# Performance work log

Hardware: AMD Instinct MI355X
Metric: run time of the kernel (lower is better)

## Reference

```python
import jax, jax.numpy as jnp
import numpy as np
from jax import lax

EPS = 1e-31
V, L, B, T = 30000, 400, 16, 145
E, EH, DH, ENC, COMB = 100, 150, 200, 300, 500
SOS = 1


def setup_inputs() -> dict:
    key = jax.random.key(0)
    ks = jax.random.split(key, 32)
    def p(i, shape):
        return jax.random.normal(ks[i], shape, dtype=jnp.float32) * 0.05
    return {
        "input_tensor": jax.random.randint(ks[0], (L, B), 0, V),
        "embedding": p(1, (V, E)),
        "enc_Wih_f": p(2, (3 * EH, E)), "enc_Whh_f": p(3, (3 * EH, EH)),
        "enc_bih_f": p(4, (3 * EH,)), "enc_bhh_f": p(5, (3 * EH,)),
        "enc_Wih_b": p(6, (3 * EH, E)), "enc_Whh_b": p(7, (3 * EH, EH)),
        "enc_bih_b": p(8, (3 * EH,)), "enc_bhh_b": p(9, (3 * EH,)),
        "adapter_W": p(10, (DH, ENC)), "adapter_b": p(11, (DH,)),
        "dec_Wih": p(12, (3 * DH, E)), "dec_Whh": p(13, (3 * DH, DH)),
        "dec_bih": p(14, (3 * DH,)), "dec_bhh": p(15, (3 * DH,)),
        "bil_W": p(16, (1, DH, ENC)), "bil_b": p(17, (1,)),
        "cover_weight": jax.random.uniform(ks[18], (1,), dtype=jnp.float32),
        "ptr_W": p(19, (1, COMB)), "ptr_b": p(20, (1,)),
        "preout_W": p(21, (E, COMB)), "preout_b": p(22, (E,)),
        "out_b": p(23, (V,)),
    }


def _gru_cell(x, h, Wih, Whh, bih, bhh):
    # torch GRU cell semantics (gates ordered r, z, n)
    gi = x @ Wih.T + bih
    gh = h @ Whh.T + bhh
    ir, iz, i_n = jnp.split(gi, 3, axis=-1)
    hr, hz, hn = jnp.split(gh, 3, axis=-1)
    r = jax.nn.sigmoid(ir + hr)
    z = jax.nn.sigmoid(iz + hz)
    n = jnp.tanh(i_n + r * hn)
    return (1.0 - z) * n + z * h


def _run_gru(emb, Wih, Whh, bih, bhh):
    # emb: [L, B, E] -> outputs [L, B, H], final hidden [B, H]
    h0 = jnp.zeros((emb.shape[1], Whh.shape[1]), emb.dtype)
    def step(h, x):
        h = _gru_cell(x, h, Wih, Whh, bih, bhh)
        return h, h
    hT, ys = lax.scan(step, h0, emb)
    return ys, hT


def reference(input_tensor, embedding,
              enc_Wih_f, enc_Whh_f, enc_bih_f, enc_bhh_f,
              enc_Wih_b, enc_Whh_b, enc_bih_b, enc_bhh_b,
              adapter_W, adapter_b,
              dec_Wih, dec_Whh, dec_bih, dec_bhh,
              bil_W, bil_b, cover_weight,
              ptr_W, ptr_b, preout_W, preout_b, out_b):
    # ----- encoder: bidirectional single-layer GRU -----
    emb = embedding[input_tensor]                       # [L, B, E]
    out_f, h_f = _run_gru(emb, enc_Wih_f, enc_Whh_f, enc_bih_f, enc_bhh_f)
    out_r, h_b = _run_gru(emb[::-1], enc_Wih_b, enc_Whh_b, enc_bih_b, enc_bhh_b)
    enc_out = jnp.concatenate([out_f, out_r[::-1]], axis=-1)   # [L, B, 300]
    enc_hidden = jnp.concatenate([h_f, h_b], axis=-1)          # [B, 300]
    h0 = enc_hidden @ adapter_W.T + adapter_b                  # enc_dec_adapter -> [B, 200]

    enc_word_idx = input_tensor.T                              # [B, L]
    batch_idx = jnp.arange(enc_out.shape[1])[:, None]

    # ----- decoder: greedy loop with enc attention + coverage + pointer-gen -----
    def dec_step(carry, _):
        h, cover, tok = carry
        x = embedding[tok]                                     # [B, E]
        h = _gru_cell(x, h, dec_Wih, dec_Whh, dec_bih, dec_bhh)
        # bilinear energy: h W e + b, plus coverage term
        hW = h @ bil_W[0]                                      # [B, 300]
        energy = jnp.einsum('be,lbe->lb', hW, enc_out) + bil_b[0]
        energy = energy + cover_weight[0] * jnp.log(cover.T + EPS)
        attn = jax.nn.softmax(energy, axis=0)                  # [L, B], softmax over enc steps
        context = jnp.einsum('lbe,lb->be', enc_out, attn)      # [B, 300]
        combined = jnp.concatenate([h, context], axis=-1)      # [B, 500]
        pre = combined @ preout_W.T + preout_b                 # [B, 100]
        logits = pre @ embedding.T + out_b                     # tied output embedding [B, V]
        p_ptr = jax.nn.sigmoid(combined @ ptr_W.T + ptr_b)     # [B, 1]
        gen = jax.nn.softmax(logits, axis=1)
        attn_bl = attn.T                                       # [B, L]
        out = (1.0 - p_ptr) * gen
        out = out.at[batch_idx, enc_word_idx].add(p_ptr * attn_bl)
        new_tok = jnp.argmax(out, axis=1)
        return (h, cover + attn_bl, new_tok), out

    cover0 = jnp.zeros(enc_word_idx.shape, emb.dtype)
    tok0 = jnp.full((enc_out.shape[1],), SOS, dtype=input_tensor.dtype)
    _, outputs = lax.scan(dec_step, (h0, cover0, tok0), None, length=T)
    return outputs  # [T, B, V] pointer-generator mixture probabilities
```

## Files before the change

### kernel.cpp

```cpp
#include <hip/hip_runtime.h>

namespace {

constexpr int Vv=30000, Ll=400, Bb=16, Tt=145;
constexpr int Ee=100, EHh=150, DHh=200, ENc=300;
constexpr int SOS_TOK=1;
constexpr int NB=256, NT=512;

constexpr long SO_EMB = 0;
constexpr long SO_GIF = SO_EMB + 6400L*100;
constexpr long SO_GIB = SO_GIF + 6400L*450;
constexpr long SO_ENC = SO_GIB + 6400L*450;
constexpr long SO_WCAT= SO_GIF;

constexpr long OFF_M    = 0;
constexpr long OFF_N    = OFF_M + 6400L*200;
constexpr long OFF_Q    = OFF_N + 6400L*100;
constexpr long OFF_HENC = OFF_Q + 6400;
constexpr long OFF_HDEC = OFF_HENC + 2L*16*150;
constexpr long OFF_COVER= OFF_HDEC + 2L*16*200;
constexpr long OFF_EXPE = OFF_COVER + 6400;
constexpr long OFF_CTXP = OFF_EXPE + 2L*6400;
constexpr long OFF_PRE  = OFF_CTXP + 2L*16*8*104;
constexpr long OFF_PPTR = OFF_PRE + 2L*16*100;
constexpr long OFF_ZATT = OFF_PPTR + 32;
constexpr long OFF_PSUM = OFF_ZATT + 32;
constexpr long OFF_CAND = OFF_PSUM + 2L*4096;
constexpr long WS_F32_END = OFF_CAND + 2L*16*400*2;
constexpr long PMAX_BYTE = ((WS_F32_END*4 + 255)/256)*256;
constexpr long IWS_BYTE  = PMAX_BYTE + 2L*4096*8;
constexpr int ISVL=0, IGV=6400, IGLS=12800, ICG0=19216, INGR=23328;
constexpr long BAR_BYTE  = ((IWS_BYTE + 23344L*4 + 255)/256)*256;
constexpr int HB_CNT=0, HB_GEN=32, EP_H=64, EP_CTX=96, EP_PRE=128, EP_S4=160, ABRT=192;

struct Args {
  const int* itok;
  const float* emb;
  const float* Wfih; const float* Wfhh; const float* bfih; const float* bfhh;
  const float* Wbih; const float* Wbhh; const float* bbih; const float* bbhh;
  const float* adW; const float* adb;
  const float* dWih; const float* dWhh; const float* dbih; const float* dbhh;
  const float* bilW; const float* bilb; const float* cw;
  const float* ptrW; const float* ptrb;
  const float* preW; const float* preb; const float* outb;
  float* out; float* ws; unsigned long long* pmax; int* iws; int* bar;
};

__device__ __forceinline__ int chunkStart(int c){ return c*117 + (c<48? c:48); }
__device__ __forceinline__ int chunkSize(int c){ return 117 + (c<48?1:0); }
__device__ __forceinline__ float sigm(float x){ return 1.f/(1.f+expf(-x)); }
__device__ __forceinline__ unsigned long long packvi(float val, int v){
  return ((unsigned long long)__float_as_uint(val)<<32) | (unsigned)(~(unsigned)v);
}
__device__ __forceinline__ float ald(const float* p){
  return __hip_atomic_load(p, __ATOMIC_RELAXED, __HIP_MEMORY_SCOPE_AGENT); }
__device__ __forceinline__ void ast(float* p, float v){
  __hip_atomic_store(p, v, __ATOMIC_RELAXED, __HIP_MEMORY_SCOPE_AGENT); }
__device__ __forceinline__ unsigned long long aldu(const unsigned long long* p){
  return __hip_atomic_load(p, __ATOMIC_RELAXED, __HIP_MEMORY_SCOPE_AGENT); }
__device__ __forceinline__ void astu(unsigned long long* p, unsigned long long v){
  __hip_atomic_store(p, v, __ATOMIC_RELAXED, __HIP_MEMORY_SCOPE_AGENT); }
__device__ __forceinline__ int aldi(const int* p){
  return __hip_atomic_load(p, __ATOMIC_RELAXED, __HIP_MEMORY_SCOPE_AGENT); }

#define CTXP_PTR(par,b,g2,k) (a.ws + OFF_CTXP + (((long)(par)*16+(b))*8+(g2))*104 + (k))

__device__ __forceinline__ void hbar(int* bar){
  __syncthreads();
  if (threadIdx.x==0){
    int* cnt=bar+HB_CNT; int* gen=bar+HB_GEN; int* abrt=bar+ABRT;
    if (aldi(abrt)==0){
      __builtin_amdgcn_fence(__ATOMIC_RELEASE, "agent");
      int g = aldi(gen);
      int arr = __hip_atomic_fetch_add(cnt, 1, __ATOMIC_RELAXED, __HIP_MEMORY_SCOPE_AGENT);
      if (arr == NB-1){
        __hip_atomic_store(cnt, 0, __ATOMIC_RELAXED, __HIP_MEMORY_SCOPE_AGENT);
        __hip_atomic_fetch_add(gen, 1, __ATOMIC_RELEASE, __HIP_MEMORY_SCOPE_AGENT);
      } else {
        long it=0;
        while (aldi(gen) == g){
          __builtin_amdgcn_s_sleep(2);
          if (++it > 3000000L){ __hip_atomic_store(abrt,1,__ATOMIC_RELAXED,__HIP_MEMORY_SCOPE_AGENT); break; }
          if ((it&1023)==0 && aldi(abrt)!=0) break;
        }
      }
      __builtin_amdgcn_fence(__ATOMIC_ACQUIRE, "agent");
    }
  }
  __syncthreads();
}

__device__ __forceinline__ void waitEp(int* ep, int target, int* abrt){
  if (threadIdx.x==0){
    if (aldi(abrt)==0){
      long it=0;
      while (aldi(ep) < target){
        __builtin_amdgcn_s_sleep(1);
        if (++it > 3000000L){ __hip_atomic_store(abrt,1,__ATOMIC_RELAXED,__HIP_MEMORY_SCOPE_AGENT); break; }
        if ((it&2047)==0 && aldi(abrt)!=0) break;
      }
    }
  }
  __syncthreads();
}
__device__ __forceinline__ void bumpEp(int* ep){
  __syncthreads();
  if (threadIdx.x==0){
    asm volatile("s_waitcnt vmcnt(0) lgkmcnt(0)" ::: "memory");
    __hip_atomic_fetch_add(ep, 1, __ATOMIC_RELAXED, __HIP_MEMORY_SCOPE_AGENT);
  }
}

__device__ void sortB(const Args& a, int b, char* smem){
  int tid=threadIdx.x;
  int* key=(int*)smem;
  key[tid] = (tid<Ll)? (a.itok[tid*16+b]*Ll + tid) : 0x7FFFFFFF;
  __syncthreads();
  for (int k=2;k<=512;k<<=1){
    for (int j=k>>1;j>0;j>>=1){
      int ixj = tid^j;
      if (ixj>tid){
        int x=key[tid], y=key[ixj];
        bool up = ((tid&k)==0);
        if ((x>y)==up){ key[tid]=y; key[ixj]=x; }
      }
      __syncthreads();
    }
  }
  int* ngS=(int*)(smem+2048);
  if (tid==0){
    int* svl=a.iws+ISVL+b*400; int* gvv=a.iws+IGV+b*400;
    int* gls=a.iws+IGLS+b*401;
    int ng=0, prev=-1;
    for (int i=0;i<400;i++){
      int kk=key[i]; int tok=kk/400, l=kk-tok*400;
      svl[i]=l;
      if (tok!=prev){ gvv[ng]=tok; gls[ng]=i; ng++; prev=tok; }
    }
    gls[ng]=400;
    a.iws[INGR+b]=ng;
    ngS[0]=ng;
  }
  __syncthreads();
  int ng=ngS[0];
  const int* gvv=a.iws+IGV+b*400;
  for (int c=tid;c<=256;c+=NT){
    int target=(c<256)? chunkStart(c) : 0x7FFFFFFF;
    int lo=0,hi=ng;
    while(lo<hi){ int mid=(lo+hi)>>1; if (gvv[mid]<target) lo=mid+1; else hi=mid; }
    a.iws[ICG0+b*257+c]=lo;
  }
}

template<int MODE>
__device__ void tileGemm(const Args& a, char* smem){
  float* Xl=(float*)smem;
  float* Wl=(float*)(smem+25600);
  const int K   = MODE? 300 : 100;
  const int NC  = MODE? 301 : 900;
  const int nCT = MODE? 5 : 15;
  const int nTiles = 100*nCT;
  const float* X = a.out + (MODE? SO_ENC : SO_EMB);
  int ty=threadIdx.x>>4, tx=threadIdx.x&15;
  for (int tile=blockIdx.x; tile<nTiles; tile+=NB){
    int rt=tile%100, ct=tile/100;
    int r0=rt*64, c0=ct*64;
    float acc[2][4];
    #pragma unroll
    for (int i=0;i<2;i++){
      #pragma unroll
      for (int j=0;j<4;j++) acc[i][j]=0.f;
    }
    for (int k0=0;k0<K;k0+=100){
      for (int i=threadIdx.x;i<1600;i+=NT){
        int rr=i/25, e4=i%25;
        ((float4*)Xl)[rr*25+e4] = *((const float4*)(X + (long)(r0+rr)*K + k0) + e4);
      }
      for (int i=threadIdx.x;i<1600;i+=NT){
        int rr=i/25, e4=i%25; int c=c0+rr;
        float4 w={0.f,0.f,0.f,0.f};
        if (c<NC){
          const float* wr;
          if (MODE==0) wr = (c<450)? (a.Wfih + (long)c*100) : (a.Wbih + (long)(c-450)*100);
          else         wr = a.out + SO_WCAT + (long)c*300 + k0;
          w = *((const float4*)wr + e4);
        }
        ((float4*)Wl)[rr*25+e4]=w;
      }
      __syncthreads();
      for (int k4=0;k4<25;k4++){
        float4 a4[2], b4[4];
        #pragma unroll
        for (int i=0;i<2;i++) a4[i]=((float4*)Xl)[(ty*2+i)*25+k4];
        #pragma unroll
        for (int j=0;j<4;j++) b4[j]=((float4*)Wl)[(tx*4+j)*25+k4];
        #pragma unroll
        for (int i=0;i<2;i++){
          #pragma unroll
          for (int j=0;j<4;j++){
            acc[i][j] += a4[i].x*b4[j].x;
            acc[i][j] += a4[i].y*b4[j].y;
            acc[i][j] += a4[i].z*b4[j].z;
            acc[i][j] += a4[i].w*b4[j].w;
          }
        }
      }
      __syncthreads();
    }
    #pragma unroll
    for (int i=0;i<2;i++){
      #pragma unroll
      for (int j=0;j<4;j++){
        int r=r0+ty*2+i, c=c0+tx*4+j;
        if (c<NC){
          if (MODE==0){
            int dir=c/450, cc=c-dir*450;
            float v=acc[i][j] + (dir? a.bbih : a.bfih)[cc];
            a.out[(dir?SO_GIB:SO_GIF) + (long)r*450 + cc]=v;
          } else {
            if (c<200)      a.ws[OFF_M + (long)r*200 + c]=acc[i][j];
            else if (c<300) a.ws[OFF_N + (long)r*100 + (c-200)]=acc[i][j];
            else            a.ws[OFF_Q + r]=acc[i][j];
          }
        }
      }
    }
  }
}

__device__ void encoderPhase(const Args& a, int bid, char* smem){
  int tid=threadIdx.x;
  int dir=bid>>4, b=bid&15;
  float* hbuf=(float*)smem;
  float* gbuf=(float*)(smem+2048);
  float* pacc=(float*)(smem+8192);
  const float* Whh = dir? a.Wbhh : a.Wfhh;
  const float* bhh = dir? a.bbhh : a.bfhh;
  const float* giBase = a.out + (dir? SO_GIB : SO_GIF);
  int ks=tid/150; int j=tid-ks*150;
  bool act = (ks<3);
  float w[3][50];
  if (act){
    #pragma unroll
    for (int g=0;g<3;g++)
      for (int k=0;k<50;k++)
        w[g][k]=Whh[(long)(g*150+j)*150 + ks*50 + k];
  }
  float b0=0,b1=0,b2=0;
  if (act && ks==0){ b0=bhh[j]; b1=bhh[150+j]; b2=bhh[300+j]; }
  for (int i=tid;i<192;i+=NT) hbuf[i]=0.f;
  {
    int l0 = dir? 399 : 0;
    for (int i=tid;i<450;i+=NT) gbuf[i]=giBase[((long)l0*16+b)*450+i];
  }
  __syncthreads();
  for (int s=0;s<400;s++){
    int p=s&1;
    int l=dir? 399-s : s;
    if (tid>=450 && s+1<400){
      int ln=dir? 399-(s+1) : s+1;
      for (int i=tid-450;i<450;i+=62) gbuf[(p^1)*452+i]=giBase[((long)ln*16+b)*450+i];
    }
    if (act){
      float ar=0.f, az=0.f, an=0.f;
      const float* hr=hbuf + p*192 + ks*64;
      #pragma unroll
      for (int k4=0;k4<12;k4++){
        float4 h4=*(const float4*)(hr + k4*4);
        ar+=h4.x*w[0][k4*4+0]; ar+=h4.y*w[0][k4*4+1]; ar+=h4.z*w[0][k4*4+2]; ar+=h4.w*w[0][k4*4+3];
        az+=h4.x*w[1][k4*4+0]; az+=h4.y*w[1][k4*4+1]; az+=h4.z*w[1][k4*4+2]; az+=h4.w*w[1][k4*4+3];
        an+=h4.x*w[2][k4*4+0]; an+=h4.y*w[2][k4*4+1]; an+=h4.z*w[2][k4*4+2]; an+=h4.w*w[2][k4*4+3];
      }
      {
        float h48=hr[48], h49=hr[49];
        ar+=h48*w[0][48]+h49*w[0][49];
        az+=h48*w[1][48]+h49*w[1][49];
        an+=h48*w[2][48]+h49*w[2][49];
      }
      pacc[(ks*3+0)*152+j]=ar;
      pacc[(ks*3+1)*152+j]=az;
      pacc[(ks*3+2)*152+j]=an;
    }
    __syncthreads();
    if (act && ks==0){
      float ar=pacc[(0*3+0)*152+j]+pacc[(1*3+0)*152+j]+pacc[(2*3+0)*152+j];
      float az=pacc[(0*3+1)*152+j]+pacc[(1*3+1)*152+j]+pacc[(2*3+1)*152+j];
      float an=pacc[(0*3+2)*152+j]+pacc[(1*3+2)*152+j]+pacc[(2*3+2)*152+j];
      const float* gi=gbuf + p*452;
      float r=sigm(gi[j]      + ar + b0);
      float z=sigm(gi[150+j]  + az + b1);
      float n=tanhf(gi[300+j] + r*(an + b2));
      int slot=(j/50)*64 + (j%50);
      float hold=hbuf[p*192+slot];
      float hv=(1.f-z)*n + z*hold;
      hbuf[(p^1)*192+slot]=hv;
      a.out[SO_ENC + ((long)l*16+b)*300 + dir*150 + j]=hv;
      if (s==399) a.ws[OFF_HENC + ((long)dir*16+b)*150 + j]=hv;
    }
    __syncthreads();
  }
}

__device__ void s1Phase(const Args& a, int bid, int t, char* smem){
  int tid=threadIdx.x;
  int q=t&1, p1=q^1;
  float* xw=(float*)smem;
  float* hw=(float*)(smem+6400);
  int* tokL=(int*)(smem+19200);
  if (t==0){
    if (tid<16) tokL[tid]=SOS_TOK;
  } else {
    int b=tid>>5, ln=tid&31;
    float zs=0.f;
    for (int c=ln;c<256;c+=32) zs+=ald(&a.ws[OFF_PSUM + ((long)p1*256+c)*16 + b]);
    #pragma unroll
    for (int off=16;off;off>>=1) zs+=__shfl_xor(zs,off,32);
    float Z=zs;
    unsigned long long best=0;
    for (int c=ln;c<256;c+=32){
      unsigned long long pm=aldu(&a.pmax[((long)p1*256+c)*16+b]);
      float ev=__uint_as_float((unsigned)(pm>>32));
      int v=(int)(~(unsigned)(pm & 0xFFFFFFFFull));
      unsigned long long pk=packvi(ev/Z, v);
      if (pk>best) best=pk;
    }
    int ng=a.iws[INGR+b];
    const float* cd=a.ws+OFF_CAND + ((long)p1*16+b)*800;
    const int* gvv=a.iws+IGV+b*400;
    for (int g=ln;g<ng;g+=32){
      float v1=ald(&cd[g*2]), v2=ald(&cd[g*2+1]);
      unsigned long long pk=packvi(v1/Z + v2, gvv[g]);
      if (pk>best) best=pk;
    }
    #pragma unroll
    for (int off=16;off;off>>=1){
      unsigned long long o=__shfl_xor(best,off,32);
      if (o>best) best=o;
    }
    if (ln==0) tokL[b]=(int)(~(unsigned)(best & 0xFFFFFFFFull));
  }
  __syncthreads();
  for (int i=tid;i<1600;i+=NT){ int b=i/100, e=i-b*100; xw[i]=a.emb[(long)tokL[b]*100+e]; }
  for (int i=tid;i<3200;i+=NT) hw[i]=ald(&a.ws[OFF_HDEC + (long)p1*3200 + i]);
  __syncthreads();
  int pair=tid>>3, lane=tid&7;
  int uj=pair>>4, b=pair&15;
  int j=bid*4+uj;
  float air=0,aiz=0,ain=0,ahr=0,ahz=0,ahn=0;
  const float* x=xw+b*100;
  for (int k=lane;k<100;k+=8){
    float xv=x[k];
    air+=xv*a.dWih[(long)j*100+k];
    aiz+=xv*a.dWih[(long)(200+j)*100+k];
    ain+=xv*a.dWih[(long)(400+j)*100+k];
  }
  const float* h=hw+b*200;
  for (int k=lane;k<200;k+=8){
    float hv=h[k];
    ahr+=hv*a.dWhh[(long)j*200+k];
    ahz+=hv*a.dWhh[(long)(200+j)*200+k];
    ahn+=hv*a.dWhh[(long)(400+j)*200+k];
  }
  #pragma unroll
  for (int off=4;off;off>>=1){
    air+=__shfl_xor(air,off,8); aiz+=__shfl_xor(aiz,off,8); ain+=__shfl_xor(ain,off,8);
    ahr+=__shfl_xor(ahr,off,8); ahz+=__shfl_xor(ahz,off,8); ahn+=__shfl_xor(ahn,off,8);
  }
  if (lane==0){
    float r=sigm(air + a.dbih[j]     + ahr + a.dbhh[j]);
    float z=sigm(aiz + a.dbih[200+j] + ahz + a.dbhh[200+j]);
    float n=tanhf(ain + a.dbih[400+j] + r*(ahn + a.dbhh[400+j]));
    ast(&a.ws[OFF_HDEC + (long)q*3200 + b*200 + j], (1.f-z)*n + z*h[j]);
  }
}

__device__ void s2ePhase(const Args& a, int idx, int t, char* smem){
  int tid=threadIdx.x;
  int q=t&1, p1=q^1;
  int b=idx&15, lg=idx>>4, l0=lg*50;
  float* hb =(float*)smem;
  float* exl=(float*)(smem+1024);
  float* zpS=(float*)(smem+1280);
  for (int i=tid;i<200;i+=NT) hb[i]=ald(&a.ws[OFF_HDEC + (long)q*3200 + b*200 + i]);
  if (tid==0){
    float zp=0.f;
    if (t>0){
      #pragma unroll
      for (int g2=0;g2<8;g2++) zp+=ald(CTXP_PTR(p1,b,g2,101));
    }
    zpS[0]=zp;
  }
  __syncthreads();
  int unit=tid>>3, lane=tid&7;
  if (unit<50){
    int l=l0+unit;
    const float* Mr=a.ws+OFF_M + (long)(l*16+b)*200;
    float acc=0.f;
    for (int k=lane;k<200;k+=8) acc+=hb[k]*Mr[k];
    #pragma unroll
    for (int off=4;off;off>>=1) acc+=__shfl_xor(acc,off,8);
    if (lane==0){
      float* cov=a.ws+OFF_COVER + b*400 + l;
      float cv=*cov;
      if (t>0) cv += ald(&a.ws[OFF_EXPE + (long)p1*6400 + l*16 + b]) / zpS[0];
      *cov=cv;
      float en = acc + a.bilb[0] + a.cw[0]*logf(cv + 1e-31f);
      float ex = expf(en);
      ast(&a.ws[OFF_EXPE + (long)q*6400 + l*16 + b], ex);
      exl[unit]=ex;
    }
  }
  __syncthreads();
  int u2=tid>>2, lane2=tid&3;
  if (u2<102){
    int k=u2; float acc=0.f;
    if (k<100){
      for (int ll=lane2;ll<50;ll+=4) acc+=exl[ll]*a.ws[OFF_N + (long)((l0+ll)*16+b)*100 + k];
    } else if (k==100){
      for (int ll=lane2;ll<50;ll+=4) acc+=exl[ll]*a.ws[OFF_Q + (l0+ll)*16 + b];
    } else {
      for (int ll=lane2;ll<50;ll+=4) acc+=exl[ll];
    }
    #pragma unroll
    for (int off=2;off;off>>=1) acc+=__shfl_xor(acc,off,4);
    if (lane2==0) ast(CTXP_PTR(q,b,lg,k), acc);
  }
}

__device__ void preFinal(const Args& a, int b, int t, char* smem, int* bar){
  int tid=threadIdx.x;
  int q=t&1;
  float* hb   =(float*)smem;
  float* prehL=(float*)(smem+1024);
  float* ctxs =(float*)(smem+1536);
  for (int i=tid;i<200;i+=NT) hb[i]=ald(&a.ws[OFF_HDEC + (long)q*3200 + b*200 + i]);
  __syncthreads();
  int unit=tid>>2, lane=tid&3;
  if (unit<101){
    const float* w=(unit<100)? (a.preW + (long)unit*500) : a.ptrW;
    float acc=0.f;
    for (int k=lane;k<200;k+=4) acc+=hb[k]*w[k];
    #pragma unroll
    for (int off=2;off;off>>=1) acc+=__shfl_xor(acc,off,4);
    if (lane==0) prehL[unit]=acc;
  }
  waitEp(bar+EP_CTX, 128*(t+1), bar+ABRT);
  if (tid<408){
    int k=tid>>2, lane2=tid&3;
    float acc=0.f;
    for (int g2=lane2;g2<8;g2+=4) acc+=ald(CTXP_PTR(q,b,g2,k));
    #pragma unroll
    for (int off=2;off;off>>=1) acc+=__shfl_xor(acc,off,4);
    if (lane2==0) ctxs[k]=acc;
  }
  __syncthreads();
  if (tid<100){
    int k=tid;
    ast(&a.ws[OFF_PRE + ((long)q*16+b)*100 + k], ctxs[k]/ctxs[101] + prehL[k] + a.preb[k]);
  }
  if (tid==511){
    float za=ctxs[101];
    ast(&a.ws[OFF_ZATT + (long)q*16 + b], za);
    ast(&a.ws[OFF_PPTR + (long)q*16 + b], sigm(ctxs[100]/za + prehL[100] + a.ptrb[0]));
  }
}

__device__ void wbPhase(const Args& a, int c, int p1, int tr, float* exPrev, char* smem){
  int tid=threadIdx.x;
  int v0=chunkStart(c), nv=chunkSize(c);
  float* zpart=(float*)(smem+8192);
  float* zl1=(float*)(smem+10240);
  float* pp1=(float*)(smem+10304);
  {
    int b=tid&15, seg=tid>>4;
    float z=0.f;
    for (int cc=seg;cc<256;cc+=32) z+=ald(&a.ws[OFF_PSUM + ((long)p1*256+cc)*16 + b]);
    zpart[seg*16+b]=z;
  }
  __syncthreads();
  if (tid<16){
    float z=0.f;
    for (int s2=0;s2<32;s2++) z+=zpart[s2*16+tid];
    zl1[tid]=z;
    pp1[tid]=ald(&a.ws[OFF_PPTR + (long)p1*16 + tid]);
  }
  __syncthreads();
  if (tid<16){
    int b=tid;
    float sc=(1.f-pp1[b])/zl1[b];
    const int* cg0=a.iws+ICG0+b*257; const int* gvv=a.iws+IGV+b*400;
    const float* cd=a.ws+OFF_CAND + ((long)p1*16+b)*800;
    for (int g=cg0[c];g<cg0[c+1];g++){
      int idx=(gvv[g]-v0)*17+b;
      exPrev[idx] += ald(&cd[g*2+1])*(1.f-pp1[b])/sc;
    }
  }
  __syncthreads();
  {
    int tot=nv*16;
    for (int u=tid;u<tot;u+=NT){
      int b2=u/nv, vl=u-b2*nv;
      float sc=(1.f-pp1[b2])/zl1[b2];
      __builtin_nontemporal_store(exPrev[vl*17+b2]*sc,
                                  &a.out[((long)tr*16+b2)*30000 + v0+vl]);
    }
  }
  __syncthreads();
}

__device__ void s4Main(const Args& a, int c, int q, float* exCur, char* smem){
  int tid=threadIdx.x;
  int v0=chunkStart(c), nv=chunkSize(c);
  float* preL=(float*)smem;
  float* ppqL=(float*)(smem+6400);
  float* zaqL=(float*)(smem+6464);
  for (int u=tid;u<1600;u+=NT){
    int b=u/100, k=u-b*100;
    preL[u]=ald(&a.ws[OFF_PRE + ((long)q*16+b)*100 + k]);
  }
  if (tid<16){
    ppqL[tid]=ald(&a.ws[OFF_PPTR + (long)q*16 + tid]);
    zaqL[tid]=ald(&a.ws[OFF_ZATT + (long)q*16 + tid]);
  }
  __syncthreads();
  int bloc=tid&15;
  float4 preg[25];
  {
    const float4* p4=(const float4*)(preL + bloc*100);
    #pragma unroll
    for (int e4=0;e4<25;e4++) preg[e4]=p4[e4];
  }
  int nu=nv*16;
  const float4* emb4=(const float4*)a.emb;
  for (int u=tid;u<nu;u+=NT){
    int vl=u>>4; int v=v0+vl;
    float acc=a.outb[v];
    const float4* er=emb4 + (long)v*25;
    #pragma unroll
    for (int e4=0;e4<25;e4++){
      float4 A=er[e4], Bv=preg[e4];
      acc += A.x*Bv.x + A.y*Bv.y + A.z*Bv.z + A.w*Bv.w;
    }
    exCur[vl*17+bloc]=expf(acc);
  }
  __syncthreads();
  {
    int b=tid>>5, sg=tid&31;
    float s=0.f; unsigned long long m=0;
    for (int vl=sg;vl<nv;vl+=32){
      float ex=exCur[vl*17+b];
      s+=ex;
      unsigned long long pk=packvi(ex, v0+vl);
      if (pk>m) m=pk;
    }
    #pragma unroll
    for (int off=16;off;off>>=1){
      s+=__shfl_xor(s,off,32);
      unsigned long long om=__shfl_xor(m,off,32);
      if (om>m) m=om;
    }
    if (sg==0){
      ast(&a.ws[OFF_PSUM + ((long)q*256+c)*16 + b], s);
      astu(&a.pmax[((long)q*256+c)*16 + b], m);
    }
  }
  if (tid<16){
    int b=tid;
    const int* cg0=a.iws+ICG0+b*257; const int* gvv=a.iws+IGV+b*400;
    const int* gls=a.iws+IGLS+b*401; const int* svl=a.iws+ISVL+b*400;
    float* cd=a.ws+OFF_CAND + ((long)q*16+b)*800;
    float pfac=ppqL[b]/(1.f-ppqL[b]);
    for (int g=cg0[c];g<cg0[c+1];g++){
      int v=gvv[g];
      float gs=0.f;
      for (int i2=gls[g];i2<gls[g+1];i2++) gs+=ald(&a.ws[OFF_EXPE + (long)q*6400 + svl[i2]*16 + b]);
      ast(&cd[g*2],   exCur[(v-v0)*17+b]);
      ast(&cd[g*2+1], pfac*gs/zaqL[b]);
    }
  }
}

__global__ void kInitBar(int* bar){
  int t=threadIdx.x;
  if (t<256) bar[t]=0;
}

__global__ __launch_bounds__(NT,1) void mega(Args a){
  __shared__ __align__(16) char smem[53248];
  int bid=blockIdx.x, tid=threadIdx.x;
  int* bar=a.bar;
  int* abrt=bar+ABRT;
  float* exBuf0=(float*)(smem+36864);
  float* exBuf1=(float*)(smem+44928);

  if (bid<16){
    sortB(a,bid,smem);
  } else {
    for (long i=(long)(bid-16)*NT+tid; i<640000; i+=240L*NT){
      long pair=i/100; int e=(int)(i-pair*100);
      a.out[SO_EMB+i]=a.emb[(long)a.itok[pair]*100+e];
    }
    for (int i=(bid-16)*NT+tid; i<6400; i+=240*NT) a.ws[OFF_COVER+i]=0.f;
  }
  hbar(bar);

  tileGemm<0>(a,smem);
  hbar(bar);

  if (bid<32) encoderPhase(a,bid,smem);
  hbar(bar);

  for (long i=(long)bid*NT+tid; i<90300; i+=(long)NB*NT){
    int rr=(int)(i/300), k=(int)(i-(long)rr*300);
    float v;
    if (rr<200)      v=a.bilW[(long)rr*300+k];
    else if (rr<300) v=a.preW[(long)(rr-200)*500+200+k];
    else             v=a.ptrW[200+k];
    a.out[SO_WCAT+i]=v;
  }
  if (bid>=32 && bid<48){
    int b=bid-32;
    int unit=tid>>1, lane=tid&1;
    if (unit<200){
      int j=unit;
      const float* w=a.adW+(long)j*300 + lane*150;
      const float* hh=a.ws+OFF_HENC + ((long)lane*16+b)*150;
      float acc=0.f;
      for (int e=0;e<150;e++) acc+=hh[e]*w[e];
      acc+=__shfl_xor(acc,1,2);
      if (lane==0) a.ws[OFF_HDEC + 1L*3200 + b*200 + j]=acc + a.adb[j];
    }
  }
  hbar(bar);

  tileGemm<1>(a,smem);
  hbar(bar);

  for (int t=0;t<Tt;t++){
    int q=t&1, p1=q^1;
    float* exPrev = p1? exBuf1 : exBuf0;
    float* exCur  = q?  exBuf1 : exBuf0;
    if (bid<50){
      waitEp(bar+EP_S4, 256*t, abrt);
      s1Phase(a,bid,t,smem);
      bumpEp(bar+EP_H);
    }
    if (t>0) wbPhase(a,bid,p1,t-1,exPrev,smem);
    if (bid>=64 && bid<192){
      waitEp(bar+EP_H, 50*(t+1), abrt);
      s2ePhase(a,bid-64,t,smem);
      bumpEp(bar+EP_CTX);
    }
    if (bid>=240){
      waitEp(bar+EP_H, 50*(t+1), abrt);
      preFinal(a,bid-240,t,smem,bar);
      bumpEp(bar+EP_PRE);
    }
    waitEp(bar+EP_PRE, 16*(t+1), abrt);
    s4Main(a,bid,q,exCur,smem);
    bumpEp(bar+EP_S4);
  }
  waitEp(bar+EP_S4, 256*Tt, abrt);
  wbPhase(a,bid,(Tt-1)&1,Tt-1,((Tt-1)&1)?exBuf1:exBuf0,smem);
}

}

extern "C" void kernel_launch(void* const* d_in, const int* in_sizes, int n_in,
                              void* d_out, int out_size, void* d_ws, size_t ws_size,
                              hipStream_t stream) {
  Args a;
  a.itok=(const int*)d_in[0];
  a.emb =(const float*)d_in[1];
  a.Wfih=(const float*)d_in[2]; a.Wfhh=(const float*)d_in[3];
  a.bfih=(const float*)d_in[4]; a.bfhh=(const float*)d_in[5];
  a.Wbih=(const float*)d_in[6]; a.Wbhh=(const float*)d_in[7];
  a.bbih=(const float*)d_in[8]; a.bbhh=(const float*)d_in[9];
  a.adW =(const float*)d_in[10]; a.adb=(const float*)d_in[11];
  a.dWih=(const float*)d_in[12]; a.dWhh=(const float*)d_in[13];
  a.dbih=(const float*)d_in[14]; a.dbhh=(const float*)d_in[15];
  a.bilW=(const float*)d_in[16]; a.bilb=(const float*)d_in[17];
  a.cw  =(const float*)d_in[18];
  a.ptrW=(const float*)d_in[19]; a.ptrb=(const float*)d_in[20];
  a.preW=(const float*)d_in[21]; a.preb=(const float*)d_in[22];
  a.outb=(const float*)d_in[23];
  a.out =(float*)d_out;
  a.ws  =(float*)d_ws;
  a.pmax=(unsigned long long*)((char*)d_ws + PMAX_BYTE);
  a.iws =(int*)((char*)d_ws + IWS_BYTE);
  a.bar =(int*)((char*)d_ws + BAR_BYTE);

  kInitBar<<<dim3(1),dim3(256),0,stream>>>(a.bar);
  void* kargs[] = { (void*)&a };
  hipLaunchCooperativeKernel(reinterpret_cast<const void*>(mega),
                             dim3(NB), dim3(NT), kargs, 0, stream);
}
```

Baseline: 11.36 ms.

## Replace double-buffered decoder scratch with per-step ring slots and drop preFinal stage

Per-step intermediates (hidden state, exp energies, context partials, psum/pmax, candidates) now go into a ring of per-timestep slots. Most slots live in not-yet-written regions of the output buffer, so they are never overwritten across steps and plain loads can replace relaxed atomic loads. The separate preFinal block group is removed. The pre/ptr projection of h moves into s1, and the context reduction is folded into s4 and wb, which removes one epoch-wait stage from the critical path. It also adds exponential backoff in the spin-wait and relies on reusing output memory as scratch before it is finally written.

Measured after the change: 12.38 ms. 1.09x slower.

```diff
diff --git a/kernel.cpp b/kernel.cpp
--- a/kernel.cpp
+++ b/kernel.cpp
@@ -13,25 +13,28 @@
 constexpr long SO_ENC = SO_GIB + 6400L*450;
 constexpr long SO_WCAT= SO_GIF;
 
+constexpr int RH    = 0;
+constexpr int REXP  = 3200;
+constexpr int RCTX  = 9600;
+constexpr int RPREH = 22912;
+constexpr int RPSUM = 24576;
+constexpr int RPMAX = 28672;
+constexpr int RCAND = 36864;
+constexpr int RING_SZ = 49664;
+
 constexpr long OFF_M    = 0;
 constexpr long OFF_N    = OFF_M + 6400L*200;
 constexpr long OFF_Q    = OFF_N + 6400L*100;
 constexpr long OFF_HENC = OFF_Q + 6400;
-constexpr long OFF_HDEC = OFF_HENC + 2L*16*150;
-constexpr long OFF_COVER= OFF_HDEC + 2L*16*200;
-constexpr long OFF_EXPE = OFF_COVER + 6400;
-constexpr long OFF_CTXP = OFF_EXPE + 2L*6400;
-constexpr long OFF_PRE  = OFF_CTXP + 2L*16*8*104;
-constexpr long OFF_PPTR = OFF_PRE + 2L*16*100;
-constexpr long OFF_ZATT = OFF_PPTR + 32;
-constexpr long OFF_PSUM = OFF_ZATT + 32;
-constexpr long OFF_CAND = OFF_PSUM + 2L*4096;
-constexpr long WS_F32_END = OFF_CAND + 2L*16*400*2;
-constexpr long PMAX_BYTE = ((WS_F32_END*4 + 255)/256)*256;
-constexpr long IWS_BYTE  = PMAX_BYTE + 2L*4096*8;
+constexpr long OFF_H0   = OFF_HENC + 4800;
+constexpr long OFF_COVER= OFF_H0 + 3200;
+constexpr long OFF_R143 = OFF_COVER + 8192;
+constexpr long OFF_R144 = OFF_R143 + RING_SZ;
+constexpr long WS_F32_END = OFF_R144 + RING_SZ;
+constexpr long IWS_BYTE  = ((WS_F32_END*4 + 255)/256)*256;
 constexpr int ISVL=0, IGV=6400, IGLS=12800, ICG0=19216, INGR=23328;
 constexpr long BAR_BYTE  = ((IWS_BYTE + 23344L*4 + 255)/256)*256;
-constexpr int HB_CNT=0, HB_GEN=32, EP_H=64, EP_CTX=96, EP_PRE=128, EP_S4=160, ABRT=192;
+constexpr int HB_CNT=0, HB_GEN=32, EP_H=64, EP_CTX=96, EP_S4=128, EP_SET=160, ABRT=192;
 
 struct Args {
   const int* itok;
@@ -43,7 +46,7 @@
   const float* bilW; const float* bilb; const float* cw;
   const float* ptrW; const float* ptrb;
   const float* preW; const float* preb; const float* outb;
-  float* out; float* ws; unsigned long long* pmax; int* iws; int* bar;
+  float* out; float* ws; int* iws; int* bar;
 };
 
 __device__ __forceinline__ int chunkStart(int c){ return c*117 + (c<48? c:48); }
@@ -52,18 +55,17 @@
 __device__ __forceinline__ unsigned long long packvi(float val, int v){
   return ((unsigned long long)__float_as_uint(val)<<32) | (unsigned)(~(unsigned)v);
 }
-__device__ __forceinline__ float ald(const float* p){
-  return __hip_atomic_load(p, __ATOMIC_RELAXED, __HIP_MEMORY_SCOPE_AGENT); }
 __device__ __forceinline__ void ast(float* p, float v){
   __hip_atomic_store(p, v, __ATOMIC_RELAXED, __HIP_MEMORY_SCOPE_AGENT); }
-__device__ __forceinline__ unsigned long long aldu(const unsigned long long* p){
-  return __hip_atomic_load(p, __ATOMIC_RELAXED, __HIP_MEMORY_SCOPE_AGENT); }
 __device__ __forceinline__ void astu(unsigned long long* p, unsigned long long v){
   __hip_atomic_store(p, v, __ATOMIC_RELAXED, __HIP_MEMORY_SCOPE_AGENT); }
 __device__ __forceinline__ int aldi(const int* p){
   return __hip_atomic_load(p, __ATOMIC_RELAXED, __HIP_MEMORY_SCOPE_AGENT); }
 
-#define CTXP_PTR(par,b,g2,k) (a.ws + OFF_CTXP + (((long)(par)*16+(b))*8+(g2))*104 + (k))
+__device__ __forceinline__ float* ringBase(const Args& a, int t){
+  if (t<=142) return a.out + (long)(t+2)*480000;
+  return a.ws + (t==143 ? OFF_R143 : OFF_R144);
+}
 
 __device__ __forceinline__ void hbar(int* bar){
   __syncthreads();
@@ -80,7 +82,7 @@
         long it=0;
         while (aldi(gen) == g){
           __builtin_amdgcn_s_sleep(2);
-          if (++it > 3000000L){ __hip_atomic_store(abrt,1,__ATOMIC_RELAXED,__HIP_MEMORY_SCOPE_AGENT); break; }
+          if (++it > 2000000L){ __hip_atomic_store(abrt,1,__ATOMIC_RELAXED,__HIP_MEMORY_SCOPE_AGENT); break; }
           if ((it&1023)==0 && aldi(abrt)!=0) break;
         }
       }
@@ -95,10 +97,11 @@
     if (aldi(abrt)==0){
       long it=0;
       while (aldi(ep) < target){
-        __builtin_amdgcn_s_sleep(1);
-        if (++it > 3000000L){ __hip_atomic_store(abrt,1,__ATOMIC_RELAXED,__HIP_MEMORY_SCOPE_AGENT); break; }
-        if ((it&2047)==0 && aldi(abrt)!=0) break;
-      }
+        if (it<32) __builtin_amdgcn_s_sleep(1); else __builtin_amdgcn_s_sleep(8);
+        if (++it > 2000000L){ __hip_atomic_store(abrt,1,__ATOMIC_RELAXED,__HIP_MEMORY_SCOPE_AGENT); break; }
+        if ((it&1023)==0 && aldi(abrt)!=0) break;
+      }
+      __builtin_amdgcn_fence(__ATOMIC_ACQUIRE, "workgroup");
     }
   }
   __syncthreads();
@@ -301,35 +304,35 @@
   }
 }
 
-__device__ void s1Phase(const Args& a, int bid, int t, char* smem){
+__device__ void s1Phase(const Args& a, int bid, int t, float* slot, const float* slotP, char* smem){
   int tid=threadIdx.x;
-  int q=t&1, p1=q^1;
   float* xw=(float*)smem;
   float* hw=(float*)(smem+6400);
   int* tokL=(int*)(smem+19200);
   if (t==0){
     if (tid<16) tokL[tid]=SOS_TOK;
   } else {
+    const float* psum = slotP + RPSUM;
+    const unsigned long long* pmax=(const unsigned long long*)(slotP + RPMAX);
     int b=tid>>5, ln=tid&31;
     float zs=0.f;
-    for (int c=ln;c<256;c+=32) zs+=ald(&a.ws[OFF_PSUM + ((long)p1*256+c)*16 + b]);
+    for (int c=ln;c<256;c+=32) zs += psum[b*256+c];
     #pragma unroll
     for (int off=16;off;off>>=1) zs+=__shfl_xor(zs,off,32);
     float Z=zs;
     unsigned long long best=0;
     for (int c=ln;c<256;c+=32){
-      unsigned long long pm=aldu(&a.pmax[((long)p1*256+c)*16+b]);
+      unsigned long long pm=pmax[b*256+c];
       float ev=__uint_as_float((unsigned)(pm>>32));
       int v=(int)(~(unsigned)(pm & 0xFFFFFFFFull));
       unsigned long long pk=packvi(ev/Z, v);
       if (pk>best) best=pk;
     }
     int ng=a.iws[INGR+b];
-    const float* cd=a.ws+OFF_CAND + ((long)p1*16+b)*800;
+    const float* cd=slotP + RCAND + b*800;
     const int* gvv=a.iws+IGV+b*400;
     for (int g=ln;g<ng;g+=32){
-      float v1=ald(&cd[g*2]), v2=ald(&cd[g*2+1]);
-      unsigned long long pk=packvi(v1/Z + v2, gvv[g]);
+      unsigned long long pk=packvi(cd[g*2]/Z + cd[g*2+1], gvv[g]);
       if (pk>best) best=pk;
     }
     #pragma unroll
@@ -341,54 +344,72 @@
   }
   __syncthreads();
   for (int i=tid;i<1600;i+=NT){ int b=i/100, e=i-b*100; xw[i]=a.emb[(long)tokL[b]*100+e]; }
-  for (int i=tid;i<3200;i+=NT) hw[i]=ald(&a.ws[OFF_HDEC + (long)p1*3200 + i]);
-  __syncthreads();
-  int pair=tid>>3, lane=tid&7;
-  int uj=pair>>4, b=pair&15;
-  int j=bid*4+uj;
-  float air=0,aiz=0,ain=0,ahr=0,ahz=0,ahn=0;
-  const float* x=xw+b*100;
-  for (int k=lane;k<100;k+=8){
-    float xv=x[k];
-    air+=xv*a.dWih[(long)j*100+k];
-    aiz+=xv*a.dWih[(long)(200+j)*100+k];
-    ain+=xv*a.dWih[(long)(400+j)*100+k];
-  }
-  const float* h=hw+b*200;
-  for (int k=lane;k<200;k+=8){
-    float hv=h[k];
-    ahr+=hv*a.dWhh[(long)j*200+k];
-    ahz+=hv*a.dWhh[(long)(200+j)*200+k];
-    ahn+=hv*a.dWhh[(long)(400+j)*200+k];
-  }
-  #pragma unroll
-  for (int off=4;off;off>>=1){
-    air+=__shfl_xor(air,off,8); aiz+=__shfl_xor(aiz,off,8); ain+=__shfl_xor(ain,off,8);
-    ahr+=__shfl_xor(ahr,off,8); ahz+=__shfl_xor(ahz,off,8); ahn+=__shfl_xor(ahn,off,8);
-  }
-  if (lane==0){
-    float r=sigm(air + a.dbih[j]     + ahr + a.dbhh[j]);
-    float z=sigm(aiz + a.dbih[200+j] + ahz + a.dbhh[200+j]);
-    float n=tanhf(ain + a.dbih[400+j] + r*(ahn + a.dbhh[400+j]));
-    ast(&a.ws[OFF_HDEC + (long)q*3200 + b*200 + j], (1.f-z)*n + z*h[j]);
-  }
-}
-
-__device__ void s2ePhase(const Args& a, int idx, int t, char* smem){
+  const float* hprev = (t==0)? (a.ws+OFF_H0) : (slotP+RH);
+  for (int i=tid;i<3200;i+=NT) hw[i]=hprev[i];
+  __syncthreads();
+  {
+    int pair=tid>>3, lane=tid&7;
+    int uj=pair>>4, b=pair&15;
+    int j=bid*4+uj;
+    float air=0,aiz=0,ain=0,ahr=0,ahz=0,ahn=0;
+    const float* x=xw+b*100;
+    for (int k=lane;k<100;k+=8){
+      float xv=x[k];
+      air+=xv*a.dWih[(long)j*100+k];
+      aiz+=xv*a.dWih[(long)(200+j)*100+k];
+      ain+=xv*a.dWih[(long)(400+j)*100+k];
+    }
+    const float* h=hw+b*200;
+    for (int k=lane;k<200;k+=8){
+      float hv=h[k];
+      ahr+=hv*a.dWhh[(long)j*200+k];
+      ahz+=hv*a.dWhh[(long)(200+j)*200+k];
+      ahn+=hv*a.dWhh[(long)(400+j)*200+k];
+    }
+    #pragma unroll
+    for (int off=4;off;off>>=1){
+      air+=__shfl_xor(air,off,8); aiz+=__shfl_xor(aiz,off,8); ain+=__shfl_xor(ain,off,8);
+      ahr+=__shfl_xor(ahr,off,8); ahz+=__shfl_xor(ahz,off,8); ahn+=__shfl_xor(ahn,off,8);
+    }
+    if (lane==0){
+      float r=sigm(air + a.dbih[j]     + ahr + a.dbhh[j]);
+      float z=sigm(aiz + a.dbih[200+j] + ahz + a.dbhh[200+j]);
+      float n=tanhf(ain + a.dbih[400+j] + r*(ahn + a.dbhh[400+j]));
+      ast(slot + RH + b*200 + j, (1.f-z)*n + z*h[j]);
+    }
+  }
+  {
+    int nrows=(bid==49)?3:2;
+    int unit=tid>>3, lane=tid&7;
+    int jsub=unit>>4, b=unit&15;
+    if (jsub<nrows){
+      int j=bid*2+jsub;
+      const float* w=(j<100)? (a.preW + (long)j*500) : a.ptrW;
+      const float* h=hw+b*200;
+      float acc=0.f;
+      for (int k=lane;k<200;k+=8) acc+=h[k]*w[k];
+      #pragma unroll
+      for (int off=4;off;off>>=1) acc+=__shfl_xor(acc,off,8);
+      if (lane==0) ast(slot + RPREH + b*104 + j, acc);
+    }
+  }
+}
+
+__device__ void s2ePhase(const Args& a, int idx, int t, float* slot, const float* slotP, char* smem){
   int tid=threadIdx.x;
-  int q=t&1, p1=q^1;
   int b=idx&15, lg=idx>>4, l0=lg*50;
   float* hb =(float*)smem;
   float* exl=(float*)(smem+1024);
-  float* zpS=(float*)(smem+1280);
-  for (int i=tid;i<200;i+=NT) hb[i]=ald(&a.ws[OFF_HDEC + (long)q*3200 + b*200 + i]);
+  float* zaS=(float*)(smem+1280);
+  const float* hsrc=slot + RH + b*200;
+  for (int i=tid;i<200;i+=NT) hb[i]=hsrc[i];
   if (tid==0){
-    float zp=0.f;
+    float za=0.f;
     if (t>0){
       #pragma unroll
-      for (int g2=0;g2<8;g2++) zp+=ald(CTXP_PTR(p1,b,g2,101));
-    }
-    zpS[0]=zp;
+      for (int g2=0;g2<8;g2++) za += slotP[RCTX + (b*8+g2)*104 + 101];
+    }
+    zaS[0]=za;
   }
   __syncthreads();
   int unit=tid>>3, lane=tid&7;
@@ -400,13 +421,13 @@
     #pragma unroll
     for (int off=4;off;off>>=1) acc+=__shfl_xor(acc,off,8);
     if (lane==0){
-      float* cov=a.ws+OFF_COVER + b*400 + l;
+      float* cov=a.ws+OFF_COVER + (b*8+lg)*64 + unit;
       float cv=*cov;
-      if (t>0) cv += ald(&a.ws[OFF_EXPE + (long)p1*6400 + l*16 + b]) / zpS[0];
+      if (t>0) cv += slotP[REXP + b*400 + l] / zaS[0];
       *cov=cv;
       float en = acc + a.bilb[0] + a.cw[0]*logf(cv + 1e-31f);
       float ex = expf(en);
-      ast(&a.ws[OFF_EXPE + (long)q*6400 + l*16 + b], ex);
+      ast(slot + REXP + b*400 + l, ex);
       exl[unit]=ex;
     }
   }
@@ -423,76 +444,44 @@
     }
     #pragma unroll
     for (int off=2;off;off>>=1) acc+=__shfl_xor(acc,off,4);
-    if (lane2==0) ast(CTXP_PTR(q,b,lg,k), acc);
-  }
-}
-
-__device__ void preFinal(const Args& a, int b, int t, char* smem, int* bar){
-  int tid=threadIdx.x;
-  int q=t&1;
-  float* hb   =(float*)smem;
-  float* prehL=(float*)(smem+1024);
-  float* ctxs =(float*)(smem+1536);
-  for (int i=tid;i<200;i+=NT) hb[i]=ald(&a.ws[OFF_HDEC + (long)q*3200 + b*200 + i]);
-  __syncthreads();
-  int unit=tid>>2, lane=tid&3;
-  if (unit<101){
-    const float* w=(unit<100)? (a.preW + (long)unit*500) : a.ptrW;
-    float acc=0.f;
-    for (int k=lane;k<200;k+=4) acc+=hb[k]*w[k];
-    #pragma unroll
-    for (int off=2;off;off>>=1) acc+=__shfl_xor(acc,off,4);
-    if (lane==0) prehL[unit]=acc;
-  }
-  waitEp(bar+EP_CTX, 128*(t+1), bar+ABRT);
-  if (tid<408){
-    int k=tid>>2, lane2=tid&3;
-    float acc=0.f;
-    for (int g2=lane2;g2<8;g2+=4) acc+=ald(CTXP_PTR(q,b,g2,k));
-    #pragma unroll
-    for (int off=2;off;off>>=1) acc+=__shfl_xor(acc,off,4);
-    if (lane2==0) ctxs[k]=acc;
-  }
-  __syncthreads();
-  if (tid<100){
-    int k=tid;
-    ast(&a.ws[OFF_PRE + ((long)q*16+b)*100 + k], ctxs[k]/ctxs[101] + prehL[k] + a.preb[k]);
-  }
-  if (tid==511){
-    float za=ctxs[101];
-    ast(&a.ws[OFF_ZATT + (long)q*16 + b], za);
-    ast(&a.ws[OFF_PPTR + (long)q*16 + b], sigm(ctxs[100]/za + prehL[100] + a.ptrb[0]));
-  }
-}
-
-__device__ void wbPhase(const Args& a, int c, int p1, int tr, float* exPrev, char* smem){
+    if (lane2==0) ast(slot + RCTX + (b*8+lg)*104 + k, acc);
+  }
+}
+
+__device__ void wbPhase(const Args& a, int c, int tr, const float* slotP, float* exPrev, char* smem){
   int tid=threadIdx.x;
   int v0=chunkStart(c), nv=chunkSize(c);
   float* zpart=(float*)(smem+8192);
   float* zl1=(float*)(smem+10240);
   float* pp1=(float*)(smem+10304);
+  const float* psum = slotP + RPSUM;
   {
     int b=tid&15, seg=tid>>4;
     float z=0.f;
-    for (int cc=seg;cc<256;cc+=32) z+=ald(&a.ws[OFF_PSUM + ((long)p1*256+cc)*16 + b]);
+    for (int cc=seg;cc<256;cc+=32) z+=psum[b*256+cc];
     zpart[seg*16+b]=z;
-  }
-  __syncthreads();
-  if (tid<16){
-    float z=0.f;
-    for (int s2=0;s2<32;s2++) z+=zpart[s2*16+tid];
-    zl1[tid]=z;
-    pp1[tid]=ald(&a.ws[OFF_PPTR + (long)p1*16 + tid]);
   }
   __syncthreads();
   if (tid<16){
     int b=tid;
-    float sc=(1.f-pp1[b])/zl1[b];
+    float z=0.f;
+    for (int s2=0;s2<32;s2++) z+=zpart[s2*16+b];
+    zl1[b]=z;
+    float za1=0.f, qc1=0.f;
+    #pragma unroll
+    for (int g2=0;g2<8;g2++){
+      za1+=slotP[RCTX + (b*8+g2)*104 + 101];
+      qc1+=slotP[RCTX + (b*8+g2)*104 + 100];
+    }
+    pp1[b]=sigm(qc1/za1 + slotP[RPREH + b*104 + 100] + a.ptrb[0]);
+  }
+  __syncthreads();
+  if (tid<16){
+    int b=tid;
     const int* cg0=a.iws+ICG0+b*257; const int* gvv=a.iws+IGV+b*400;
-    const float* cd=a.ws+OFF_CAND + ((long)p1*16+b)*800;
+    const float* cd=slotP + RCAND + b*800;
     for (int g=cg0[c];g<cg0[c+1];g++){
-      int idx=(gvv[g]-v0)*17+b;
-      exPrev[idx] += ald(&cd[g*2+1])*(1.f-pp1[b])/sc;
+      exPrev[(gvv[g]-v0)*17+b] += cd[g*2+1]*zl1[b];
     }
   }
   __syncthreads();
@@ -508,19 +497,30 @@
   __syncthreads();
 }
 
-__device__ void s4Main(const Args& a, int c, int q, float* exCur, char* smem){
+__device__ void s4Phase(const Args& a, int c, int t, float* slot, float* exCur, char* smem){
   int tid=threadIdx.x;
   int v0=chunkStart(c), nv=chunkSize(c);
   float* preL=(float*)smem;
-  float* ppqL=(float*)(smem+6400);
-  float* zaqL=(float*)(smem+6464);
+  float* zaL =(float*)(smem+6400);
+  float* ppqL=(float*)(smem+6464);
+  if (tid<16){
+    int b=tid;
+    float za=0.f, qc=0.f;
+    #pragma unroll
+    for (int g2=0;g2<8;g2++){
+      za+=slot[RCTX + (b*8+g2)*104 + 101];
+      qc+=slot[RCTX + (b*8+g2)*104 + 100];
+    }
+    zaL[b]=za;
+    ppqL[b]=sigm(qc/za + slot[RPREH + b*104 + 100] + a.ptrb[0]);
+  }
+  __syncthreads();
   for (int u=tid;u<1600;u+=NT){
     int b=u/100, k=u-b*100;
-    preL[u]=ald(&a.ws[OFF_PRE + ((long)q*16+b)*100 + k]);
-  }
-  if (tid<16){
-    ppqL[tid]=ald(&a.ws[OFF_PPTR + (long)q*16 + tid]);
-    zaqL[tid]=ald(&a.ws[OFF_ZATT + (long)q*16 + tid]);
+    float sv=0.f;
+    #pragma unroll
+    for (int g2=0;g2<8;g2++) sv+=slot[RCTX + (b*8+g2)*104 + k];
+    preL[u]=sv/zaL[b] + slot[RPREH + b*104 + k] + a.preb[k];
   }
   __syncthreads();
   int bloc=tid&15;
@@ -560,22 +560,22 @@
       if (om>m) m=om;
     }
     if (sg==0){
-      ast(&a.ws[OFF_PSUM + ((long)q*256+c)*16 + b], s);
-      astu(&a.pmax[((long)q*256+c)*16 + b], m);
+      ast(slot + RPSUM + b*256 + c, s);
+      astu((unsigned long long*)(slot + RPMAX) + b*256 + c, m);
     }
   }
   if (tid<16){
     int b=tid;
     const int* cg0=a.iws+ICG0+b*257; const int* gvv=a.iws+IGV+b*400;
     const int* gls=a.iws+IGLS+b*401; const int* svl=a.iws+ISVL+b*400;
-    float* cd=a.ws+OFF_CAND + ((long)q*16+b)*800;
+    float* cd=slot + RCAND + b*800;
     float pfac=ppqL[b]/(1.f-ppqL[b]);
     for (int g=cg0[c];g<cg0[c+1];g++){
       int v=gvv[g];
       float gs=0.f;
-      for (int i2=gls[g];i2<gls[g+1];i2++) gs+=ald(&a.ws[OFF_EXPE + (long)q*6400 + svl[i2]*16 + b]);
-      ast(&cd[g*2],   exCur[(v-v0)*17+b]);
-      ast(&cd[g*2+1], pfac*gs/zaqL[b]);
+      for (int i2=gls[g];i2<gls[g+1];i2++) gs+=slot[REXP + b*400 + svl[i2]];
+      ast(cd+g*2,   exCur[(v-v0)*17+b]);
+      ast(cd+g*2+1, pfac*gs/zaL[b]);
     }
   }
 }
@@ -600,7 +600,7 @@
       long pair=i/100; int e=(int)(i-pair*100);
       a.out[SO_EMB+i]=a.emb[(long)a.itok[pair]*100+e];
     }
-    for (int i=(bid-16)*NT+tid; i<6400; i+=240*NT) a.ws[OFF_COVER+i]=0.f;
+    for (int i=(bid-16)*NT+tid; i<8192; i+=240*NT) a.ws[OFF_COVER+i]=0.f;
   }
   hbar(bar);
 
@@ -628,40 +628,40 @@
       float acc=0.f;
       for (int e=0;e<150;e++) acc+=hh[e]*w[e];
       acc+=__shfl_xor(acc,1,2);
-      if (lane==0) a.ws[OFF_HDEC + 1L*3200 + b*200 + j]=acc + a.adb[j];
+      if (lane==0) a.ws[OFF_H0 + b*200 + j]=acc + a.adb[j];
     }
   }
   hbar(bar);
 
   tileGemm<1>(a,smem);
   hbar(bar);
+  bumpEp(bar+EP_SET);
+  waitEp(bar+EP_SET, NB, abrt);
 
   for (int t=0;t<Tt;t++){
-    int q=t&1, p1=q^1;
-    float* exPrev = p1? exBuf1 : exBuf0;
-    float* exCur  = q?  exBuf1 : exBuf0;
+    int q=t&1;
+    float* exCur  = q? exBuf1 : exBuf0;
+    float* exPrev = q? exBuf0 : exBuf1;
+    float* slot   = ringBase(a,t);
+    float* slotP  = (t>0)? ringBase(a,t-1) : (float*)0;
     if (bid<50){
       waitEp(bar+EP_S4, 256*t, abrt);
-      s1Phase(a,bid,t,smem);
+      s1Phase(a,bid,t,slot,slotP,smem);
       bumpEp(bar+EP_H);
-    }
-    if (t>0) wbPhase(a,bid,p1,t-1,exPrev,smem);
-    if (bid>=64 && bid<192){
+    } else if (bid>=64 && bid<192){
       waitEp(bar+EP_H, 50*(t+1), abrt);
-      s2ePhase(a,bid-64,t,smem);
+      s2ePhase(a,bid-64,t,slot,slotP,smem);
       bumpEp(bar+EP_CTX);
-    }
-    if (bid>=240){
-      waitEp(bar+EP_H, 50*(t+1), abrt);
-      preFinal(a,bid-240,t,smem,bar);
-      bumpEp(bar+EP_PRE);
-    }
-    waitEp(bar+EP_PRE, 16*(t+1), abrt);
-    s4Main(a,bid,q,exCur,smem);
+    } else {
+      waitEp(bar+EP_S4, 256*t, abrt);
+    }
+    if (t>0) wbPhase(a,bid,t-1,slotP,exPrev,smem);
+    waitEp(bar+EP_CTX, 128*(t+1), abrt);
+    s4Phase(a,bid,t,slot,exCur,smem);
     bumpEp(bar+EP_S4);
   }
   waitEp(bar+EP_S4, 256*Tt, abrt);
-  wbPhase(a,bid,(Tt-1)&1,Tt-1,((Tt-1)&1)?exBuf1:exBuf0,smem);
+  wbPhase(a,bid,Tt-1,ringBase(a,Tt-1),((Tt-1)&1)?exBuf1:exBuf0,smem);
 }
 
 }
@@ -686,7 +686,6 @@
   a.outb=(const float*)d_in[23];
   a.out =(float*)d_out;
   a.ws  =(float*)d_ws;
-  a.pmax=(unsigned long long*)((char*)d_ws + PMAX_BYTE);
   a.iws =(int*)((char*)d_ws + IWS_BYTE);
   a.bar =(int*)((char*)d_ws + BAR_BYTE);
 
```
